# Kernel tuning notes

Hardware: AMD Instinct MI355X
Metric: run time of the kernel (lower is better)

## Reference

```python
import jax, jax.numpy as jnp
import numpy as np

B, T, I, H, C = 8192, 784, 1, 30, 10


def setup_inputs() -> dict:
    key = jax.random.key(0)
    ks = jax.random.split(key, 7)
    s_ih = 1.0 / np.sqrt(H)
    return {
        "x": jax.random.normal(ks[0], (B, T, I), dtype=jnp.float32),
        "W_ih": jax.random.uniform(ks[1], (H, I), jnp.float32, -s_ih, s_ih),
        "W_hh": jax.random.uniform(ks[2], (H, H), jnp.float32, -s_ih, s_ih),
        "b_ih": jax.random.uniform(ks[3], (H,), jnp.float32, -s_ih, s_ih),
        "b_hh": jax.random.uniform(ks[4], (H,), jnp.float32, -s_ih, s_ih),
        "W_fc": jax.random.uniform(ks[5], (C, H), jnp.float32, -s_ih, s_ih),
        "b_fc": jax.random.uniform(ks[6], (C,), jnp.float32, -s_ih, s_ih),
    }


def reference(x, W_ih, W_hh, b_ih, b_hh, W_fc, b_fc):
    # x: [B, T, I] -> scan over time. h_t = tanh(x_t W_ih^T + b_ih + h W_hh^T + b_hh)
    xs = jnp.swapaxes(x, 0, 1)  # [T, B, I]
    h0 = jnp.zeros((x.shape[0], W_hh.shape[0]), dtype=x.dtype)
    bias = b_ih + b_hh  # [H]

    def step(h, xt):
        h_new = jnp.tanh(xt @ W_ih.T + h @ W_hh.T + bias)
        return h_new, None

    hT, _ = jax.lax.scan(step, h0, xs)  # hT: [B, H] == out[:, -1, :]
    return hT @ W_fc.T + b_fc  # [B, C]
```

## Files before the change

### kernel.cpp

```cpp
#include <hip/hip_runtime.h>


#define BB 8192
#define TT 784
#define HH 30
#define CC 10

typedef __attribute__((ext_vector_type(8))) short  bf16x8;
typedef __attribute__((ext_vector_type(4))) float  f32x4;
typedef __attribute__((ext_vector_type(4))) unsigned uint4v;

#if __has_builtin(__builtin_amdgcn_exp2f)
#define EXP2(v) __builtin_amdgcn_exp2f(v)
#else
#define EXP2(v) __expf((v) * 0.69314718055994531f)
#endif

#define SCL 2.8853900817779268f

__device__ __forceinline__ float tanh_e2(float s) {
    return 1.0f - 2.0f * __builtin_amdgcn_rcpf(EXP2(s) + 1.0f);
}

#define BPAIR(p0, p1, hp, lp) do {                                          \
    asm("v_cvt_pk_bf16_f32 %0, %1, %2" : "=v"(hp) : "v"(p0), "v"(p1));      \
    const float _h0 = __uint_as_float((hp) << 16);                          \
    const float _h1 = __uint_as_float((hp) & 0xffff0000u);                  \
    const float _l0 = (p0) - _h0;                                           \
    const float _l1 = (p1) - _h1;                                           \
    asm("v_cvt_pk_bf16_f32 %0, %1, %2" : "=v"(lp) : "v"(_l0), "v"(_l1));    \
} while (0)

#define MFMA(A, B, C) __builtin_amdgcn_mfma_f32_16x16x32_bf16((A), (B), (C), 0, 0, 0)

__global__ __launch_bounds__(128)
__attribute__((amdgpu_waves_per_eu(1, 1)))
void rnn_scan_kernel(const float* __restrict__ x,
                     const float* __restrict__ W_ih,
                     const float* __restrict__ W_hh,
                     const float* __restrict__ b_ih,
                     const float* __restrict__ b_hh,
                     const float* __restrict__ W_fc,
                     const float* __restrict__ b_fc,
                     float* __restrict__ out) {
    __shared__ uint4v E[2][2][64];
    __shared__ float hfc[16][33];

    const int tid  = threadIdx.x;
    const int wv   = tid >> 6;
    const int lane = tid & 63;
    const int n    = lane & 15;
    const int g    = lane >> 4;
    const int b    = blockIdx.x * 16 + n;

    const int rr = 8 * (n >> 2) + (n & 3) + 4 * wv;
    unsigned ah[4], al[4];
#pragma unroll
    for (int d = 0; d < 4; ++d) {
        const int k0 = 8 * g + 2 * d, k1 = k0 + 1;
        const float wa = (rr < HH && k0 < HH) ? SCL * W_hh[rr * HH + k0] : 0.f;
        const float wb = (rr < HH && k1 < HH) ? SCL * W_hh[rr * HH + k1] : 0.f;
        const unsigned ua = __float_as_uint(wa), ub = __float_as_uint(wb);
        ah[d] = (ub & 0xffff0000u) | (ua >> 16);
        const float la = wa - __uint_as_float(ua & 0xffff0000u);
        const float lb = wb - __uint_as_float(ub & 0xffff0000u);
        al[d] = (__float_as_uint(lb) & 0xffff0000u) | (__float_as_uint(la) >> 16);
    }
    bf16x8 Ah = __builtin_bit_cast(bf16x8, (uint4v){ah[0], ah[1], ah[2], ah[3]});
    bf16x8 Al = __builtin_bit_cast(bf16x8, (uint4v){al[0], al[1], al[2], al[3]});
    asm volatile("" : "+v"(Ah), "+v"(Al));

    float bias[4], wih[4];
#pragma unroll
    for (int r = 0; r < 4; ++r) {
        const int q = 8 * g + 4 * wv + r;
        bias[r] = (q < HH) ? SCL * (b_ih[q] + b_hh[q]) : 0.f;
        wih[r]  = (q < HH) ? SCL * W_ih[q] : 0.f;
        asm volatile("" : "+v"(bias[r]), "+v"(wih[r]));
    }

    float h0 = 0.f, h1 = 0.f, h2 = 0.f, h3 = 0.f;

    const float* xp = x + (size_t)b * TT;
    const int NQ = TT / 4;
    float4 xq = *(const float4*)xp;
    float4 xn = *(const float4*)(xp + 4);

    for (int qq = 0; qq < NQ; ++qq) {
        const float4 xf = (qq + 2 < NQ) ? *(const float4*)(xp + (qq + 2) * 4)
                                        : make_float4(0.f, 0.f, 0.f, 0.f);
#pragma unroll
        for (int u = 0; u < 4; ++u) {
            const float xt = (u == 0) ? xq.x : (u == 1) ? xq.y
                           : (u == 2) ? xq.z : xq.w;
            const int p = u & 1;

            unsigned hp0, hp1, lp0, lp1;
            BPAIR(h0, h1, hp0, lp0);
            BPAIR(h2, h3, hp1, lp1);
            E[p][wv][lane] = (uint4v){hp0, hp1, lp0, lp1};

            uint4v bh, bl;
            if (wv == 0) { bh = (uint4v){hp0, hp1, 0, 0}; bl = (uint4v){lp0, lp1, 0, 0}; }
            else         { bh = (uint4v){0, 0, hp0, hp1}; bl = (uint4v){0, 0, lp0, lp1}; }
            const bf16x8 Bh = __builtin_bit_cast(bf16x8, bh);
            const bf16x8 Bl = __builtin_bit_cast(bf16x8, bl);

            f32x4 acc = { fmaf(xt, wih[0], bias[0]), fmaf(xt, wih[1], bias[1]),
                          fmaf(xt, wih[2], bias[2]), fmaf(xt, wih[3], bias[3]) };
            const f32x4 zed = {0.f, 0.f, 0.f, 0.f};
            f32x4 P0 = MFMA(Ah, Bh, acc);
            f32x4 Q0 = MFMA(Ah, Bl, zed);
            Q0 = MFMA(Al, Bh, Q0);

            __syncthreads();
            const uint4v rv = E[p][wv ^ 1][lane];
            const unsigned r0 = rv[0], r1 = rv[1], r2 = rv[2], r3 = rv[3];
            uint4v ch, cl;
            if (wv == 0) { ch = (uint4v){0, 0, r0, r1}; cl = (uint4v){0, 0, r2, r3}; }
            else         { ch = (uint4v){r0, r1, 0, 0}; cl = (uint4v){r2, r3, 0, 0}; }
            const bf16x8 Ch = __builtin_bit_cast(bf16x8, ch);
            const bf16x8 Cl = __builtin_bit_cast(bf16x8, cl);

            const f32x4 d1 = MFMA(Ah, Ch, P0);
            const f32x4 d2 = MFMA(Ah, Cl, Q0);
            const f32x4 d3 = MFMA(Al, Ch, zed);
            const f32x4 s  = (d1 + d2) + d3;

            h0 = tanh_e2(s[0]); h1 = tanh_e2(s[1]);
            h2 = tanh_e2(s[2]); h3 = tanh_e2(s[3]);
        }
        xq = xn;
        xn = xf;
    }

    hfc[n][8 * g + 4 * wv + 0] = h0;
    hfc[n][8 * g + 4 * wv + 1] = h1;
    hfc[n][8 * g + 4 * wv + 2] = h2;
    hfc[n][8 * g + 4 * wv + 3] = h3;
    __syncthreads();
    if (wv == 0) {
#pragma unroll
        for (int j = 0; j < 3; ++j) {
            const int c = g + 4 * j;
            if (c < CC) {
                float acc = b_fc[c];
#pragma unroll
                for (int k = 0; k < HH; ++k)
                    acc = fmaf(W_fc[c * HH + k], hfc[n][k], acc);
                out[(size_t)b * CC + c] = acc;
            }
        }
    }
}

extern "C" void kernel_launch(void* const* d_in, const int* in_sizes, int n_in,
                              void* d_out, int out_size, void* d_ws, size_t ws_size,
                              hipStream_t stream) {
    const float* x    = (const float*)d_in[0];
    const float* W_ih = (const float*)d_in[1];
    const float* W_hh = (const float*)d_in[2];
    const float* b_ih = (const float*)d_in[3];
    const float* b_hh = (const float*)d_in[4];
    const float* W_fc = (const float*)d_in[5];
    const float* b_fc = (const float*)d_in[6];

    hipLaunchKernelGGL(rnn_scan_kernel,
                       dim3(BB / 16), dim3(128), 0, stream,
                       x, W_ih, W_hh, b_ih, b_hh, W_fc, b_fc,
                       (float*)d_out);
}
```

Measured before the change: 301.4 us.

## Halve batch per block, double occupancy, and merge MFMA chain after exchange

Each block now processes 8 batch rows instead of 16, with the upper 8 MFMA columns wasted as duplicates, and the grid doubles. waves_per_eu is raised to 2 so two blocks can interleave their serial latency chains. The per-step MFMA sequence now waits for the LDS exchange first and then issues three full-K MFMAs instead of six split ones. This shortens the dependent MFMA chain per step and adds latency hiding, at the cost of putting the LDS barrier on the critical path before any MFMA and doubling the total MFMA work.

```diff
diff --git a/kernel.cpp b/kernel.cpp
--- a/kernel.cpp
+++ b/kernel.cpp
@@ -34,7 +34,7 @@
 #define MFMA(A, B, C) __builtin_amdgcn_mfma_f32_16x16x32_bf16((A), (B), (C), 0, 0, 0)
 
 __global__ __launch_bounds__(128)
-__attribute__((amdgpu_waves_per_eu(1, 1)))
+__attribute__((amdgpu_waves_per_eu(2, 2)))
 void rnn_scan_kernel(const float* __restrict__ x,
                      const float* __restrict__ W_ih,
                      const float* __restrict__ W_hh,
@@ -44,14 +44,15 @@
                      const float* __restrict__ b_fc,
                      float* __restrict__ out) {
     __shared__ uint4v E[2][2][64];
-    __shared__ float hfc[16][33];
+    __shared__ float hfc[8][33];
 
     const int tid  = threadIdx.x;
     const int wv   = tid >> 6;
     const int lane = tid & 63;
     const int n    = lane & 15;
     const int g    = lane >> 4;
-    const int b    = blockIdx.x * 16 + n;
+    const bool live = (n < 8);
+    const int b    = blockIdx.x * 8 + (live ? n : 0);
 
     const int rr = 8 * (n >> 2) + (n & 3) + 4 * wv;
     unsigned ah[4], al[4];
@@ -100,32 +101,25 @@
             BPAIR(h2, h3, hp1, lp1);
             E[p][wv][lane] = (uint4v){hp0, hp1, lp0, lp1};
 
+            f32x4 acc = { fmaf(xt, wih[0], bias[0]), fmaf(xt, wih[1], bias[1]),
+                          fmaf(xt, wih[2], bias[2]), fmaf(xt, wih[3], bias[3]) };
+
+            __syncthreads();
+            const uint4v rv = E[p][wv ^ 1][lane];
+
             uint4v bh, bl;
-            if (wv == 0) { bh = (uint4v){hp0, hp1, 0, 0}; bl = (uint4v){lp0, lp1, 0, 0}; }
-            else         { bh = (uint4v){0, 0, hp0, hp1}; bl = (uint4v){0, 0, lp0, lp1}; }
+            if (wv == 0) { bh = (uint4v){hp0, hp1, rv[0], rv[1]};
+                           bl = (uint4v){lp0, lp1, rv[2], rv[3]}; }
+            else         { bh = (uint4v){rv[0], rv[1], hp0, hp1};
+                           bl = (uint4v){rv[2], rv[3], lp0, lp1}; }
             const bf16x8 Bh = __builtin_bit_cast(bf16x8, bh);
             const bf16x8 Bl = __builtin_bit_cast(bf16x8, bl);
 
-            f32x4 acc = { fmaf(xt, wih[0], bias[0]), fmaf(xt, wih[1], bias[1]),
-                          fmaf(xt, wih[2], bias[2]), fmaf(xt, wih[3], bias[3]) };
             const f32x4 zed = {0.f, 0.f, 0.f, 0.f};
-            f32x4 P0 = MFMA(Ah, Bh, acc);
-            f32x4 Q0 = MFMA(Ah, Bl, zed);
-            Q0 = MFMA(Al, Bh, Q0);
-
-            __syncthreads();
-            const uint4v rv = E[p][wv ^ 1][lane];
-            const unsigned r0 = rv[0], r1 = rv[1], r2 = rv[2], r3 = rv[3];
-            uint4v ch, cl;
-            if (wv == 0) { ch = (uint4v){0, 0, r0, r1}; cl = (uint4v){0, 0, r2, r3}; }
-            else         { ch = (uint4v){r0, r1, 0, 0}; cl = (uint4v){r2, r3, 0, 0}; }
-            const bf16x8 Ch = __builtin_bit_cast(bf16x8, ch);
-            const bf16x8 Cl = __builtin_bit_cast(bf16x8, cl);
-
-            const f32x4 d1 = MFMA(Ah, Ch, P0);
-            const f32x4 d2 = MFMA(Ah, Cl, Q0);
-            const f32x4 d3 = MFMA(Al, Ch, zed);
-            const f32x4 s  = (d1 + d2) + d3;
+            acc = MFMA(Ah, Bh, acc);
+            f32x4 q1 = MFMA(Ah, Bl, zed);
+            f32x4 q2 = MFMA(Al, Bh, zed);
+            const f32x4 s = (acc + q1) + q2;
 
             h0 = tanh_e2(s[0]); h1 = tanh_e2(s[1]);
             h2 = tanh_e2(s[2]); h3 = tanh_e2(s[3]);
@@ -134,12 +128,14 @@
         xn = xf;
     }
 
-    hfc[n][8 * g + 4 * wv + 0] = h0;
-    hfc[n][8 * g + 4 * wv + 1] = h1;
-    hfc[n][8 * g + 4 * wv + 2] = h2;
-    hfc[n][8 * g + 4 * wv + 3] = h3;
+    if (live) {
+        hfc[n][8 * g + 4 * wv + 0] = h0;
+        hfc[n][8 * g + 4 * wv + 1] = h1;
+        hfc[n][8 * g + 4 * wv + 2] = h2;
+        hfc[n][8 * g + 4 * wv + 3] = h3;
+    }
     __syncthreads();
-    if (wv == 0) {
+    if (wv == 0 && live) {
 #pragma unroll
         for (int j = 0; j < 3; ++j) {
             const int c = g + 4 * j;
@@ -166,7 +162,7 @@
     const float* b_fc = (const float*)d_in[6];
 
     hipLaunchKernelGGL(rnn_scan_kernel,
-                       dim3(BB / 16), dim3(128), 0, stream,
+                       dim3(BB / 8), dim3(128), 0, stream,
                        x, W_ih, W_hh, b_ih, b_hh, W_fc, b_fc,
                        (float*)d_out);
 }
```

New measurement: 321.4 us. 1.07x slower.
